# Optimization experiments

Measured on AMD Instinct MI355X. Metric: run time of the kernel, lower is better.

Reference implementation:

```python
import jax, jax.numpy as jnp
import numpy as np

B, S, N1, N2, NS = 2048, 1024, 8192, 16384, 256
EPS = 1e-10

def setup_inputs() -> dict:
    key = jax.random.key(0)
    ks = jax.random.split(key, 12)
    t_in = jax.random.uniform(ks[0], (B,), jnp.float32)
    y_in = jax.random.uniform(ks[1], (B, S), jnp.float32)
    den_gas = jax.random.uniform(ks[2], (B, 1), jnp.float32) * 1e4
    alpha_1st = jax.random.uniform(ks[3], (N1,), jnp.float32)
    gamma_1st = jax.random.uniform(ks[4], (N1,), jnp.float32) * 50.0
    alpha_2nd = jax.random.uniform(ks[5], (N2,), jnp.float32)
    gamma_2nd = jax.random.uniform(ks[6], (N2,), jnp.float32) * 50.0
    r1_1st = jax.random.randint(ks[7], (N1,), 0, S, jnp.int32)
    p_1st = jax.random.randint(ks[8], (N1,), 0, S, jnp.int32)
    r1_2nd = jax.random.randint(ks[9], (N2,), 0, S, jnp.int32)
    r2_2nd = jax.random.randint(ks[10], (N2,), 0, S, jnp.int32)
    p_2nd = jax.random.randint(ks[11], (N2,), 0, S, jnp.int32)
    inds_surf = 512 + jnp.arange(NS, dtype=jnp.int32)  # surface species slots
    inds_mant = 768 + jnp.arange(NS, dtype=jnp.int32)  # mantle species slots
    return dict(t_in=t_in, y_in=y_in, den_gas=den_gas,
                alpha_1st=alpha_1st, gamma_1st=gamma_1st,
                alpha_2nd=alpha_2nd, gamma_2nd=gamma_2nd,
                r1_1st=r1_1st, p_1st=p_1st,
                r1_2nd=r1_2nd, r2_2nd=r2_2nd, p_2nd=p_2nd,
                inds_surf=inds_surf, inds_mant=inds_mant)

def reference(t_in, y_in, den_gas, alpha_1st, gamma_1st, alpha_2nd, gamma_2nd,
              r1_1st, p_1st, r1_2nd, r2_2nd, p_2nd, inds_surf, inds_mant):
    zeros = jnp.zeros_like(y_in)
    # medium parameters (module_med): temperature from t, den_norm from den_gas
    T = 10.0 + 5.0 * jax.nn.sigmoid(t_in)[:, None]            # [B,1]
    # rmod_1st / rmod_2nd: modified-Arrhenius rate coefficients
    rates_1st = alpha_1st[None, :] * jnp.exp(-gamma_1st[None, :] / T)      # [B,N1]
    rates_2nd = (alpha_2nd[None, :] * jnp.sqrt(T / 300.0)
                 * jnp.exp(-gamma_2nd[None, :] / T))                       # [B,N2]
    # reaction fluxes (gather)
    terms_1st = rates_1st * y_in[:, r1_1st]                                 # [B,N1]
    terms_2nd = rates_2nd * y_in[:, r1_2nd] * y_in[:, r2_2nd] * den_gas     # [B,N2]
    # surface gain / loss assemblers (gain-only and loss-only scatters)
    gain = (zeros.at[:, p_1st].add(terms_1st)
                 .at[:, p_2nd].add(terms_2nd))[:, inds_surf]
    loss = (zeros.at[:, r1_1st].add(-terms_1st)
                 .at[:, r1_2nd].add(-terms_2nd)
                 .at[:, r2_2nd].add(-terms_2nd))[:, inds_surf]
    dy_surf_gain = jnp.sum(gain, axis=-1, keepdims=True)    # [B,1] >= 0
    dy_surf_loss = -jnp.sum(loss, axis=-1, keepdims=True)   # [B,1] >= 0
    # rmod_smt: surface<->mantle transfer coefficients (three-phase)
    y_surf_tot = jnp.sum(y_in[:, inds_surf], axis=-1, keepdims=True)
    y_mant_tot = jnp.sum(y_in[:, inds_mant], axis=-1, keepdims=True)
    k_s2m = dy_surf_gain / (y_surf_tot + EPS)  # burial rate per surface species
    k_m2s = dy_surf_loss / (y_mant_tot + EPS)  # excavation rate per mantle species
    terms_s2m = k_s2m * y_in[:, inds_surf]     # [B,NS]
    terms_m2s = k_m2s * y_in[:, inds_mant]     # [B,NS]
    # full RHS: asm_smt + asm_1st + asm_2nd
    dy = (zeros
          .at[:, p_1st].add(terms_1st).at[:, r1_1st].add(-terms_1st)
          .at[:, p_2nd].add(terms_2nd)
          .at[:, r1_2nd].add(-terms_2nd).at[:, r2_2nd].add(-terms_2nd)
          .at[:, inds_surf].add(terms_m2s - terms_s2m)
          .at[:, inds_mant].add(terms_s2m - terms_m2s))
    return dy
```

## Files before the change

### kernel.cpp

```cpp
#include <hip/hip_runtime.h>
#include <hip/hip_fp16.h>

constexpr int kB  = 2048;
constexpr int kS  = 1024;
constexpr int kN1 = 8192;
constexpr int kN2 = 16384;
constexpr int kNTERM = kN1 + kN2;
constexpr int kQT    = kNTERM / 4;
constexpr int kRoles = 2*kN1 + 3*kN2;
constexpr float kEPS = 1e-10f;
constexpr int NT = 256;

constexpr int kGrpPitchE[8] = {24, 24, 24, 32, 24, 40, 24, 40};
constexpr int kGrpBase [8]  = {0, 12288, 24576, 36864, 53248, 65536, 86016, 98304};
constexpr int kEllWords     = 118784;
constexpr int kCurWords     = 8 * kS;

constexpr size_t kWsMid  = (size_t)(kCurWords + kEllWords) * 4;
constexpr size_t kWsFull = kWsMid + (size_t)kNTERM * 16;

__global__ __launch_bounds__(NT) void ell_fill(
    const float* __restrict__ a1, const float* __restrict__ g1,
    const float* __restrict__ a2, const float* __restrict__ g2,
    const int* __restrict__ r1_1, const int* __restrict__ p_1,
    const int* __restrict__ r1_2, const int* __restrict__ r2_2,
    const int* __restrict__ p_2,
    unsigned* __restrict__ cursor, unsigned* __restrict__ ell,
    float4* __restrict__ rec)
{
    int i = blockIdx.x * NT + threadIdx.x;
    if (i >= kRoles) return;
    int s, j; bool neg;
    if (i < kN1)                  { j = i;          s = p_1[j];  neg = false; }
    else if (i < 2*kN1)           { j = i - kN1;    s = r1_1[j]; neg = true;  }
    else if (i < 2*kN1 + kN2)     { int q = i - 2*kN1;         j = kN1 + q; s = p_2[q];  neg = false; }
    else if (i < 2*kN1 + 2*kN2)   { int q = i - 2*kN1 - kN2;   j = kN1 + q; s = r1_2[q]; neg = true; }
    else                          { int q = i - 2*kN1 - 2*kN2; j = kN1 + q; s = r2_2[q]; neg = true; }
    int qq = j / kQT;
    unsigned addr = (unsigned)(j - qq * kQT + 1) << 2;
    int grp = qq * 2 + (neg ? 1 : 0);
    unsigned k = atomicAdd(&cursor[grp * kS + s], 1u);
    if (k < (unsigned)kGrpPitchE[grp]) {
        unsigned w = (unsigned)kGrpBase[grp]
                   + ((k >> 3) * (unsigned)kS + (unsigned)s) * 4u + ((k >> 1) & 3u);
        ((unsigned short*)ell)[w * 2u + (k & 1u)] = (unsigned short)addr;
    }

    if (rec && i < kNTERM) {
        float4 r;
        if (i < kN1) { r.x = a1[i]; r.y = -g1[i]; r.z = __int_as_float(r1_1[i]); r.w = 0.f; }
        else { int q = i - kN1; r.x = a2[q]; r.y = -g2[q];
               r.z = __int_as_float(r1_2[q]); r.w = __int_as_float(r2_2[q]); }
        rec[i] = r;
    }
}

__device__ __forceinline__ void accum8(uint4 e, const __half2* __restrict__ t2,
                                       float& r0, float& r1)
{
    const char* tb = (const char*)t2;
    float2 f0 = __half22float2(*(const __half2*)(tb + (e.x & 0xffffu)));
    float2 f1 = __half22float2(*(const __half2*)(tb + (e.x >> 16)));
    float2 f2 = __half22float2(*(const __half2*)(tb + (e.y & 0xffffu)));
    float2 f3 = __half22float2(*(const __half2*)(tb + (e.y >> 16)));
    float2 f4 = __half22float2(*(const __half2*)(tb + (e.z & 0xffffu)));
    float2 f5 = __half22float2(*(const __half2*)(tb + (e.z >> 16)));
    float2 f6 = __half22float2(*(const __half2*)(tb + (e.w & 0xffffu)));
    float2 f7 = __half22float2(*(const __half2*)(tb + (e.w >> 16)));
    r0 += ((f0.x + f1.x) + (f2.x + f3.x)) + ((f4.x + f5.x) + (f6.x + f7.x));
    r1 += ((f0.y + f1.y) + (f2.y + f3.y)) + ((f4.y + f5.y) + (f6.y + f7.y));
}

__device__ __forceinline__ void glist2_pf(
    const uint4* __restrict__ ap, const uint4* __restrict__ an,
    uint4 ep, uint4 en, int cp, int cn, const __half2* __restrict__ t2,
    float& p0, float& p1, float& n0, float& n1)
{
    accum8(ep, t2, p0, p1);
    accum8(en, t2, n0, n1);
    int tp = (cp + 7) >> 3;
    int tn = (cn + 7) >> 3;
    int T = tp > tn ? tp : tn;
    for (int t = 1; t < T; ++t) {
        bool dp = t < tp, dn = t < tn;
        uint4 e2, e3;
        if (dp) e2 = *ap;
        if (dn) e3 = *an;
        ap += kS; an += kS;
        if (dp) accum8(e2, t2, p0, p1);
        if (dn) accum8(e3, t2, n0, n1);
    }
}

template<bool REC>
__global__ __launch_bounds__(NT, 4) void three_phase_gather8(
    const float* __restrict__ t_in, const float* __restrict__ y_in,
    const float* __restrict__ den_gas,
    const float* __restrict__ a1, const float* __restrict__ g1,
    const float* __restrict__ a2, const float* __restrict__ g2,
    const int* __restrict__ r1_1,
    const int* __restrict__ r1_2, const int* __restrict__ r2_2,
    const unsigned* __restrict__ cursor, const unsigned* __restrict__ ell,
    const float4* __restrict__ rec, float* __restrict__ dy)
{
    __shared__ float2  y2[kS];
    __shared__ __half2 terms2[kQT + 1];
    __shared__ float   red[4][8];

    const int tid = threadIdx.x;
    const int b0  = blockIdx.x * 2;

    {
        const float4* s0 = (const float4*)(y_in + (size_t)b0 * kS);
        const float4* s1 = (const float4*)(y_in + (size_t)(b0 + 1) * kS);
        float4 va = s0[tid], vb = s1[tid];
        y2[4*tid+0] = make_float2(va.x, vb.x);
        y2[4*tid+1] = make_float2(va.y, vb.y);
        y2[4*tid+2] = make_float2(va.z, vb.z);
        y2[4*tid+3] = make_float2(va.w, vb.w);
    }
    if (tid == 0) terms2[0] = __halves2half2(__float2half(0.f), __float2half(0.f));

    float T0 = 10.f + 5.f / (1.f + __expf(-t_in[b0]));
    float T1 = 10.f + 5.f / (1.f + __expf(-t_in[b0 + 1]));
    float i0 = 1.f / T0, i1 = 1.f / T1;
    float c20 = __fsqrt_rn(T0 * (1.f / 300.f)) * den_gas[b0];
    float c21 = __fsqrt_rn(T1 * (1.f / 300.f)) * den_gas[b0 + 1];

    float acc[4][2] = {};
    float gn[2] = {}, ls[2] = {};

    #pragma unroll
    for (int q = 0; q < 4; ++q) {
        __syncthreads();
        const int base = q * kQT;
        #pragma unroll 2
        for (int it = 0; it < kQT / NT; ++it) {
            int j = base + it * NT + tid;
            float al, ng; int ra, rb;
            if (REC) {
                float4 r = rec[j];
                al = r.x; ng = r.y;
                ra = __float_as_int(r.z); rb = __float_as_int(r.w);
            } else if (j < kN1) {
                al = a1[j]; ng = -g1[j]; ra = r1_1[j]; rb = 0;
            } else {
                int u = j - kN1;
                al = a2[u]; ng = -g2[u]; ra = r1_2[u]; rb = r2_2[u];
            }
            float t0, t1;
            if (j < kN1) {
                float2 ya = y2[ra];
                t0 = al * __expf(ng * i0) * ya.x;
                t1 = al * __expf(ng * i1) * ya.y;
            } else {
                float2 ya = y2[ra], yb = y2[rb];
                t0 = c20 * al * __expf(ng * i0) * ya.x * yb.x;
                t1 = c21 * al * __expf(ng * i1) * ya.y * yb.y;
            }
            terms2[j - base + 1] = __halves2half2(__float2half(t0), __float2half(t1));
        }
        const unsigned* cp = cursor + (2*q)     * kS;
        const unsigned* cn = cursor + (2*q + 1) * kS;
        const uint4* bp = (const uint4*)(ell + kGrpBase[2*q]);
        const uint4* bn = (const uint4*)(ell + kGrpBase[2*q + 1]);
        uint4 pfp[4], pfn[4]; int ccp[4], ccn[4];
        #pragma unroll
        for (int slot = 0; slot < 4; ++slot) {
            int s = tid + slot * NT;
            int a = (int)cp[s]; ccp[slot] = a < kGrpPitchE[2*q]   ? a : kGrpPitchE[2*q];
            int b = (int)cn[s]; ccn[slot] = b < kGrpPitchE[2*q+1] ? b : kGrpPitchE[2*q+1];
            pfp[slot] = bp[s];
            pfn[slot] = bn[s];
        }
        __syncthreads();
        #pragma unroll
        for (int slot = 0; slot < 4; ++slot) {
            int s = tid + slot * NT;
            float p0 = 0.f, p1 = 0.f, n0 = 0.f, n1 = 0.f;
            glist2_pf(bp + s + kS, bn + s + kS, pfp[slot], pfn[slot],
                      ccp[slot], ccn[slot], terms2, p0, p1, n0, n1);
            acc[slot][0] += p0 - n0;
            acc[slot][1] += p1 - n1;
            if (slot == 2) { gn[0] += p0; gn[1] += p1; ls[0] += n0; ls[1] += n1; }
        }
    }

    float ys0 = y2[512 + tid].x, ys1 = y2[512 + tid].y;
    float ym0 = y2[768 + tid].x, ym1 = y2[768 + tid].y;
    float v[8] = {gn[0], ls[0], ys0, ym0, gn[1], ls[1], ys1, ym1};
    #pragma unroll
    for (int off = 32; off > 0; off >>= 1) {
        #pragma unroll
        for (int w = 0; w < 8; ++w) v[w] += __shfl_down(v[w], off, 64);
    }
    int wave = tid >> 6;
    if ((tid & 63) == 0) {
        #pragma unroll
        for (int w = 0; w < 8; ++w) red[wave][w] = v[w];
    }
    __syncthreads();
    float tv[8];
    #pragma unroll
    for (int w = 0; w < 8; ++w) tv[w] = red[0][w] + red[1][w] + red[2][w] + red[3][w];

    float ks2m0 = tv[0] / (tv[2] + kEPS), km2s0 = tv[1] / (tv[3] + kEPS);
    float ks2m1 = tv[4] / (tv[6] + kEPS), km2s1 = tv[5] / (tv[7] + kEPS);

    float* o0 = dy + (size_t)b0 * kS;
    float* o1 = o0 + kS;
    o0[tid]       = acc[0][0];
    o0[tid + 256] = acc[1][0];
    o0[tid + 512] = acc[2][0] + km2s0 * ym0 - ks2m0 * ys0;
    o0[tid + 768] = acc[3][0] + ks2m0 * ys0 - km2s0 * ym0;
    o1[tid]       = acc[0][1];
    o1[tid + 256] = acc[1][1];
    o1[tid + 512] = acc[2][1] + km2s1 * ym1 - ks2m1 * ys1;
    o1[tid + 768] = acc[3][1] + ks2m1 * ys1 - km2s1 * ym1;
}

__global__ __launch_bounds__(NT) void three_phase_scatter(
    const float* __restrict__ t_in, const float* __restrict__ y_in,
    const float* __restrict__ den_gas,
    const float* __restrict__ alpha_1st, const float* __restrict__ gamma_1st,
    const float* __restrict__ alpha_2nd, const float* __restrict__ gamma_2nd,
    const int* __restrict__ r1_1st, const int* __restrict__ p_1st,
    const int* __restrict__ r1_2nd, const int* __restrict__ r2_2nd,
    const int* __restrict__ p_2nd, float* __restrict__ dy)
{
    __shared__ float y_row[kS];
    __shared__ float accs[kS];
    __shared__ float tot[4];
    const int tid = threadIdx.x;
    const int b   = blockIdx.x;
    ((float4*)y_row)[tid] = ((const float4*)(y_in + (size_t)b * kS))[tid];
    ((float4*)accs)[tid] = make_float4(0.f, 0.f, 0.f, 0.f);
    if (tid < 4) tot[tid] = 0.f;
    float t = t_in[b];
    float T = 10.f + 5.f / (1.f + __expf(-t));
    float invT = 1.f / T, sqT = __fsqrt_rn(T * (1.f / 300.f)), dg = den_gas[b];
    __syncthreads();
    float gain = 0.f, loss = 0.f;
    for (int j = tid; j < kN1; j += NT) {
        int r1 = r1_1st[j], p = p_1st[j];
        float term = alpha_1st[j] * __expf(-gamma_1st[j] * invT) * y_row[r1];
        atomicAdd(&accs[p], term); atomicAdd(&accs[r1], -term);
        if ((unsigned)(p - 512) < 256u) gain += term;
        if ((unsigned)(r1 - 512) < 256u) loss += term;
    }
    for (int j = tid; j < kN2; j += NT) {
        int r1 = r1_2nd[j], r2 = r2_2nd[j], p = p_2nd[j];
        float term = sqT * dg * alpha_2nd[j] * __expf(-gamma_2nd[j] * invT) * y_row[r1] * y_row[r2];
        atomicAdd(&accs[p], term); atomicAdd(&accs[r1], -term); atomicAdd(&accs[r2], -term);
        if ((unsigned)(p - 512) < 256u) gain += term;
        if ((unsigned)(r1 - 512) < 256u) loss += term;
        if ((unsigned)(r2 - 512) < 256u) loss += term;
    }
    float g = gain, l = loss;
    #pragma unroll
    for (int off = 32; off > 0; off >>= 1) { g += __shfl_down(g, off, 64); l += __shfl_down(l, off, 64); }
    if ((tid & 63) == 0) { atomicAdd(&tot[0], g); atomicAdd(&tot[1], l); }
    __syncthreads();
    if (tid < 64) {
        float a2v = 0.f;
        for (int u = tid; u < 256; u += 64) a2v += y_row[512 + u];
        #pragma unroll
        for (int off = 32; off > 0; off >>= 1) a2v += __shfl_down(a2v, off, 64);
        if (tid == 0) tot[2] = a2v;
    } else if (tid < 128) {
        float m2 = 0.f;
        for (int u = tid - 64; u < 256; u += 64) m2 += y_row[768 + u];
        #pragma unroll
        for (int off = 32; off > 0; off >>= 1) m2 += __shfl_down(m2, off, 64);
        if (tid == 64) tot[3] = m2;
    }
    __syncthreads();
    float k_s2m = tot[0] / (tot[2] + kEPS);
    float k_m2s = tot[1] / (tot[3] + kEPS);
    float* out = dy + (size_t)b * kS;
    for (int s = tid; s < kS; s += NT) {
        float v = accs[s];
        if ((unsigned)(s - 512) < 256u) v += k_m2s * y_row[s + 256] - k_s2m * y_row[s];
        else if (s >= 768)              v += k_s2m * y_row[s - 256] - k_m2s * y_row[s];
        out[s] = v;
    }
}

extern "C" void kernel_launch(void* const* d_in, const int* in_sizes, int n_in,
                              void* d_out, int out_size, void* d_ws, size_t ws_size,
                              hipStream_t stream) {
    const float* t_in      = (const float*)d_in[0];
    const float* y_in      = (const float*)d_in[1];
    const float* den_gas   = (const float*)d_in[2];
    const float* alpha_1st = (const float*)d_in[3];
    const float* gamma_1st = (const float*)d_in[4];
    const float* alpha_2nd = (const float*)d_in[5];
    const float* gamma_2nd = (const float*)d_in[6];
    const int*   r1_1st    = (const int*)d_in[7];
    const int*   p_1st     = (const int*)d_in[8];
    const int*   r1_2nd    = (const int*)d_in[9];
    const int*   r2_2nd    = (const int*)d_in[10];
    const int*   p_2nd     = (const int*)d_in[11];
    float* dy = (float*)d_out;

    if (ws_size >= kWsMid) {
        unsigned* cursor = (unsigned*)d_ws;
        unsigned* ell    = cursor + kCurWords;
        float4*   rec    = (ws_size >= kWsFull)
                         ? (float4*)((char*)d_ws + kWsMid) : (float4*)nullptr;
        hipMemsetAsync(d_ws, 0, kWsMid, stream);
        ell_fill<<<kRoles / NT, NT, 0, stream>>>(
            alpha_1st, gamma_1st, alpha_2nd, gamma_2nd,
            r1_1st, p_1st, r1_2nd, r2_2nd, p_2nd, cursor, ell, rec);
        if (rec)
            three_phase_gather8<true><<<kB / 2, NT, 0, stream>>>(
                t_in, y_in, den_gas, alpha_1st, gamma_1st, alpha_2nd, gamma_2nd,
                r1_1st, r1_2nd, r2_2nd, cursor, ell, rec, dy);
        else
            three_phase_gather8<false><<<kB / 2, NT, 0, stream>>>(
                t_in, y_in, den_gas, alpha_1st, gamma_1st, alpha_2nd, gamma_2nd,
                r1_1st, r1_2nd, r2_2nd, cursor, ell, rec, dy);
    } else {
        three_phase_scatter<<<kB, NT, 0, stream>>>(
            t_in, y_in, den_gas, alpha_1st, gamma_1st, alpha_2nd, gamma_2nd,
            r1_1st, p_1st, r1_2nd, r2_2nd, p_2nd, dy);
    }
}
```

Measured before the change: 146.6 us.

## Fuse memset, ELL build and gather into one cooperative kernel with grid syncs

Merges the workspace memset, the ELL-table fill and the gather kernel into a single cooperative launch, using two grid-wide barriers between zeroing, filling and gathering. The aim is to remove two extra launches and the gaps between dependent kernels. It needs all 1024 blocks resident at once, which requires 4 blocks per CU with about 38 KB of LDS each. If the cooperative launch fails, the code falls back to the previous three-step path. Grid syncs add their own barrier cost, and the first phases run inside a kernel sized for the gather's occupancy.

```diff
diff --git a/kernel.cpp b/kernel.cpp
--- a/kernel.cpp
+++ b/kernel.cpp
@@ -1,5 +1,8 @@
 #include <hip/hip_runtime.h>
 #include <hip/hip_fp16.h>
+#include <hip/hip_cooperative_groups.h>
+
+namespace cg = cooperative_groups;
 
 constexpr int kB  = 2048;
 constexpr int kS  = 1024;
@@ -15,21 +18,19 @@
 constexpr int kGrpBase [8]  = {0, 12288, 24576, 36864, 53248, 65536, 86016, 98304};
 constexpr int kEllWords     = 118784;
 constexpr int kCurWords     = 8 * kS;
+constexpr int kZeroVecs     = (kCurWords + kEllWords) / 4;
 
 constexpr size_t kWsMid  = (size_t)(kCurWords + kEllWords) * 4;
 constexpr size_t kWsFull = kWsMid + (size_t)kNTERM * 16;
 
-__global__ __launch_bounds__(NT) void ell_fill(
-    const float* __restrict__ a1, const float* __restrict__ g1,
-    const float* __restrict__ a2, const float* __restrict__ g2,
+
+__device__ __forceinline__ void fill_role(
+    int i,
     const int* __restrict__ r1_1, const int* __restrict__ p_1,
     const int* __restrict__ r1_2, const int* __restrict__ r2_2,
     const int* __restrict__ p_2,
-    unsigned* __restrict__ cursor, unsigned* __restrict__ ell,
-    float4* __restrict__ rec)
-{
-    int i = blockIdx.x * NT + threadIdx.x;
-    if (i >= kRoles) return;
+    unsigned* __restrict__ cursor, unsigned* __restrict__ ell)
+{
     int s, j; bool neg;
     if (i < kN1)                  { j = i;          s = p_1[j];  neg = false; }
     else if (i < 2*kN1)           { j = i - kN1;    s = r1_1[j]; neg = true;  }
@@ -45,14 +46,21 @@
                    + ((k >> 3) * (unsigned)kS + (unsigned)s) * 4u + ((k >> 1) & 3u);
         ((unsigned short*)ell)[w * 2u + (k & 1u)] = (unsigned short)addr;
     }
-
-    if (rec && i < kNTERM) {
-        float4 r;
-        if (i < kN1) { r.x = a1[i]; r.y = -g1[i]; r.z = __int_as_float(r1_1[i]); r.w = 0.f; }
-        else { int q = i - kN1; r.x = a2[q]; r.y = -g2[q];
-               r.z = __int_as_float(r1_2[q]); r.w = __int_as_float(r2_2[q]); }
-        rec[i] = r;
-    }
+}
+
+__device__ __forceinline__ void fill_rec(
+    int i,
+    const float* __restrict__ a1, const float* __restrict__ g1,
+    const float* __restrict__ a2, const float* __restrict__ g2,
+    const int* __restrict__ r1_1,
+    const int* __restrict__ r1_2, const int* __restrict__ r2_2,
+    float4* __restrict__ rec)
+{
+    float4 r;
+    if (i < kN1) { r.x = a1[i]; r.y = -g1[i]; r.z = __int_as_float(r1_1[i]); r.w = 0.f; }
+    else { int q = i - kN1; r.x = a2[q]; r.y = -g2[q];
+           r.z = __int_as_float(r1_2[q]); r.w = __int_as_float(r2_2[q]); }
+    rec[i] = r;
 }
 
 __device__ __forceinline__ void accum8(uint4 e, const __half2* __restrict__ t2,
@@ -93,7 +101,7 @@
 }
 
 template<bool REC>
-__global__ __launch_bounds__(NT, 4) void three_phase_gather8(
+__device__ __forceinline__ void gather_body(
     const float* __restrict__ t_in, const float* __restrict__ y_in,
     const float* __restrict__ den_gas,
     const float* __restrict__ a1, const float* __restrict__ g1,
@@ -101,25 +109,11 @@
     const int* __restrict__ r1_1,
     const int* __restrict__ r1_2, const int* __restrict__ r2_2,
     const unsigned* __restrict__ cursor, const unsigned* __restrict__ ell,
-    const float4* __restrict__ rec, float* __restrict__ dy)
-{
-    __shared__ float2  y2[kS];
-    __shared__ __half2 terms2[kQT + 1];
-    __shared__ float   red[4][8];
-
+    const float4* __restrict__ rec, float* __restrict__ dy,
+    float2* y2, __half2* terms2, float (*red)[8])
+{
     const int tid = threadIdx.x;
     const int b0  = blockIdx.x * 2;
-
-    {
-        const float4* s0 = (const float4*)(y_in + (size_t)b0 * kS);
-        const float4* s1 = (const float4*)(y_in + (size_t)(b0 + 1) * kS);
-        float4 va = s0[tid], vb = s1[tid];
-        y2[4*tid+0] = make_float2(va.x, vb.x);
-        y2[4*tid+1] = make_float2(va.y, vb.y);
-        y2[4*tid+2] = make_float2(va.z, vb.z);
-        y2[4*tid+3] = make_float2(va.w, vb.w);
-    }
-    if (tid == 0) terms2[0] = __halves2half2(__float2half(0.f), __float2half(0.f));
 
     float T0 = 10.f + 5.f / (1.f + __expf(-t_in[b0]));
     float T1 = 10.f + 5.f / (1.f + __expf(-t_in[b0 + 1]));
@@ -219,6 +213,102 @@
     o1[tid + 768] = acc[3][1] + ks2m1 * ys1 - km2s1 * ym1;
 }
 
+template<bool REC>
+__global__ __launch_bounds__(NT, 4) void three_phase_fused(
+    const float* __restrict__ t_in, const float* __restrict__ y_in,
+    const float* __restrict__ den_gas,
+    const float* __restrict__ a1, const float* __restrict__ g1,
+    const float* __restrict__ a2, const float* __restrict__ g2,
+    const int* __restrict__ r1_1, const int* __restrict__ p_1,
+    const int* __restrict__ r1_2, const int* __restrict__ r2_2,
+    const int* __restrict__ p_2,
+    unsigned* __restrict__ cursor, unsigned* __restrict__ ell,
+    float4* __restrict__ rec, float* __restrict__ dy)
+{
+    __shared__ float2  y2[kS];
+    __shared__ __half2 terms2[kQT + 1];
+    __shared__ float   red[4][8];
+
+    const int tid = threadIdx.x;
+    const int b0  = blockIdx.x * 2;
+    const int gid = blockIdx.x * NT + tid;
+
+    {
+        const float4* s0 = (const float4*)(y_in + (size_t)b0 * kS);
+        const float4* s1 = (const float4*)(y_in + (size_t)(b0 + 1) * kS);
+        float4 va = s0[tid], vb = s1[tid];
+        y2[4*tid+0] = make_float2(va.x, vb.x);
+        y2[4*tid+1] = make_float2(va.y, vb.y);
+        y2[4*tid+2] = make_float2(va.z, vb.z);
+        y2[4*tid+3] = make_float2(va.w, vb.w);
+    }
+    if (tid == 0) terms2[0] = __halves2half2(__float2half(0.f), __float2half(0.f));
+
+    if (gid < kZeroVecs)
+        ((uint4*)cursor)[gid] = make_uint4(0u, 0u, 0u, 0u);
+
+    cg::grid_group grid = cg::this_grid();
+    grid.sync();
+
+    if (gid < kRoles)
+        fill_role(gid, r1_1, p_1, r1_2, r2_2, p_2, cursor, ell);
+    if (REC && gid < kNTERM)
+        fill_rec(gid, a1, g1, a2, g2, r1_1, r1_2, r2_2, rec);
+
+    grid.sync();
+
+    gather_body<REC>(t_in, y_in, den_gas, a1, g1, a2, g2, r1_1, r1_2, r2_2,
+                     cursor, ell, rec, dy, y2, terms2, red);
+}
+
+__global__ __launch_bounds__(NT) void ell_fill(
+    const float* __restrict__ a1, const float* __restrict__ g1,
+    const float* __restrict__ a2, const float* __restrict__ g2,
+    const int* __restrict__ r1_1, const int* __restrict__ p_1,
+    const int* __restrict__ r1_2, const int* __restrict__ r2_2,
+    const int* __restrict__ p_2,
+    unsigned* __restrict__ cursor, unsigned* __restrict__ ell,
+    float4* __restrict__ rec)
+{
+    int i = blockIdx.x * NT + threadIdx.x;
+    if (i >= kRoles) return;
+    fill_role(i, r1_1, p_1, r1_2, r2_2, p_2, cursor, ell);
+    if (rec && i < kNTERM)
+        fill_rec(i, a1, g1, a2, g2, r1_1, r1_2, r2_2, rec);
+}
+
+template<bool REC>
+__global__ __launch_bounds__(NT, 4) void three_phase_gather8(
+    const float* __restrict__ t_in, const float* __restrict__ y_in,
+    const float* __restrict__ den_gas,
+    const float* __restrict__ a1, const float* __restrict__ g1,
+    const float* __restrict__ a2, const float* __restrict__ g2,
+    const int* __restrict__ r1_1,
+    const int* __restrict__ r1_2, const int* __restrict__ r2_2,
+    const unsigned* __restrict__ cursor, const unsigned* __restrict__ ell,
+    const float4* __restrict__ rec, float* __restrict__ dy)
+{
+    __shared__ float2  y2[kS];
+    __shared__ __half2 terms2[kQT + 1];
+    __shared__ float   red[4][8];
+
+    const int tid = threadIdx.x;
+    const int b0  = blockIdx.x * 2;
+    {
+        const float4* s0 = (const float4*)(y_in + (size_t)b0 * kS);
+        const float4* s1 = (const float4*)(y_in + (size_t)(b0 + 1) * kS);
+        float4 va = s0[tid], vb = s1[tid];
+        y2[4*tid+0] = make_float2(va.x, vb.x);
+        y2[4*tid+1] = make_float2(va.y, vb.y);
+        y2[4*tid+2] = make_float2(va.z, vb.z);
+        y2[4*tid+3] = make_float2(va.w, vb.w);
+    }
+    if (tid == 0) terms2[0] = __halves2half2(__float2half(0.f), __float2half(0.f));
+
+    gather_body<REC>(t_in, y_in, den_gas, a1, g1, a2, g2, r1_1, r1_2, r2_2,
+                     cursor, ell, rec, dy, y2, terms2, red);
+}
+
 __global__ __launch_bounds__(NT) void three_phase_scatter(
     const float* __restrict__ t_in, const float* __restrict__ y_in,
     const float* __restrict__ den_gas,
@@ -308,6 +398,20 @@
         unsigned* ell    = cursor + kCurWords;
         float4*   rec    = (ws_size >= kWsFull)
                          ? (float4*)((char*)d_ws + kWsMid) : (float4*)nullptr;
+
+        void* args[] = {
+            (void*)&t_in, (void*)&y_in, (void*)&den_gas,
+            (void*)&alpha_1st, (void*)&gamma_1st, (void*)&alpha_2nd, (void*)&gamma_2nd,
+            (void*)&r1_1st, (void*)&p_1st, (void*)&r1_2nd, (void*)&r2_2nd, (void*)&p_2nd,
+            (void*)&cursor, (void*)&ell, (void*)&rec, (void*)&dy
+        };
+        const void* fn = rec ? (const void*)three_phase_fused<true>
+                             : (const void*)three_phase_fused<false>;
+        hipError_t e = hipLaunchCooperativeKernel(fn, dim3(kB / 2), dim3(NT),
+                                                  args, 0, stream);
+        if (e == hipSuccess) return;
+        (void)hipGetLastError();
+
         hipMemsetAsync(d_ws, 0, kWsMid, stream);
         ell_fill<<<kRoles / NT, NT, 0, stream>>>(
             alpha_1st, gamma_1st, alpha_2nd, gamma_2nd,
```

Measured after the change: 332.2 us. 127% more time.
